# Performance work log

Hardware: AMD Instinct MI355X
Metric: run time of the kernel (lower is better)

The kernel has to match this reference:

```python
import jax, jax.numpy as jnp
import numpy as np

N = 1_000_000
H = 128
G = 4096


def setup_inputs() -> dict:
    key = jax.random.key(0)
    k1, k2, k3, k4 = jax.random.split(key, 4)
    x = jax.random.normal(k1, (N, H), dtype=jnp.float32)
    batch = jnp.sort(jax.random.randint(k2, (N,), 0, G, dtype=jnp.int64))
    w1 = jax.random.normal(k3, (H, H), dtype=jnp.float32) * 0.05
    b1 = jnp.zeros((H,), dtype=jnp.float32)
    w2 = jax.random.normal(k4, (H, 1), dtype=jnp.float32) * 0.05
    b2 = jnp.zeros((1,), dtype=jnp.float32)
    return {"x": x, "batch": batch, "w1": w1, "b1": b1, "w2": w2, "b2": b2, "num_graphs": G}


def reference(x, batch, w1, b1, w2, b2, num_graphs):
    # attention MLP: Linear -> Tanh -> Linear(->1)
    s = (jnp.tanh(x @ w1 + b1) @ w2 + b2)[:, 0]  # [N]
    # segmented (per-graph) stable softmax
    smax = jax.ops.segment_max(s, batch, num_segments=num_graphs)  # [G]
    smax = jnp.where(jnp.isfinite(smax), smax, 0.0)  # guard empty graphs
    e = jnp.exp(s - smax[batch])  # [N]
    denom = jax.ops.segment_sum(e, batch, num_segments=num_graphs)  # [G]
    w = e / jnp.where(denom > 0, denom, 1.0)[batch]  # [N]
    # weighted sum pooling per graph -> [G, H]
    pooled = jax.ops.segment_sum(x * w[:, None], batch, num_segments=num_graphs)
    return pooled
```

## Files before the change

kernel.cpp:

```cpp
#include <hip/hip_runtime.h>
#include <math.h>

#define H 128

typedef float f32x4 __attribute__((ext_vector_type(4)));
typedef __bf16 bf16x8 __attribute__((ext_vector_type(8)));

__device__ __forceinline__ float fast_tanh(float v) {
    float e = __expf(2.0f * v);
    float r = __builtin_amdgcn_rcpf(e + 1.0f);
    return fmaf(-2.0f, r, 1.0f);
}

__global__ __launch_bounds__(512, 4) void k_compute_s_mfma(
    const float* __restrict__ x, const float* __restrict__ w1,
    const float* __restrict__ b1, const float* __restrict__ w2,
    const float* __restrict__ b2, float* __restrict__ s, int n, int ntiles)
{
    __shared__ __bf16 wsm[2 * H * H];

    const int tid = threadIdx.x;

    for (int idx = tid; idx < H * H; idx += 512) {
        int k = idx >> 7, nn = idx & 127;
        float v = w1[idx];
        __bf16 h = (__bf16)v;
        __bf16 l = (__bf16)(v - (float)h);
        int c = (k >> 3) ^ (nn & 15);
        int pos = nn * H + c * 8 + (k & 7);
        wsm[pos] = h;
        wsm[H * H + pos] = l;
    }

    const int wv = tid >> 6;
    const int lane = tid & 63;
    const int p = lane & 15;
    const int q = lane >> 4;
    const float b2v = b2[0];

    __syncthreads();

    for (int tile = blockIdx.x; tile < ntiles; tile += (int)gridDim.x) {
        const long long base = (long long)tile * 256 + wv * 32;

        bf16x8 ah[2][4], al[2][4];
        #pragma unroll
        for (int mt = 0; mt < 2; ++mt) {
            long long r = base + mt * 16 + p;
            const float4* rp = (const float4*)(x + r * H);
            const bool ok = (r < (long long)n);
            #pragma unroll
            for (int kc = 0; kc < 4; ++kc) {
                float4 u0 = {0.f, 0.f, 0.f, 0.f}, u1 = {0.f, 0.f, 0.f, 0.f};
                if (ok) { u0 = rp[kc * 8 + q * 2]; u1 = rp[kc * 8 + q * 2 + 1]; }
                float vals[8] = {u0.x, u0.y, u0.z, u0.w, u1.x, u1.y, u1.z, u1.w};
                #pragma unroll
                for (int j = 0; j < 8; ++j) {
                    __bf16 h = (__bf16)vals[j];
                    ah[mt][kc][j] = h;
                    al[mt][kc][j] = (__bf16)(vals[j] - (float)h);
                }
            }
        }

        float part[2][4] = {{0.f, 0.f, 0.f, 0.f}, {0.f, 0.f, 0.f, 0.f}};

        #pragma unroll
        for (int nt = 0; nt < 8; ++nt) {
            const int nn = nt * 16 + p;
            f32x4 acc0 = {0.f, 0.f, 0.f, 0.f};
            f32x4 acc1 = {0.f, 0.f, 0.f, 0.f};
            #pragma unroll
            for (int kc = 0; kc < 4; ++kc) {
                const int c = (kc * 4 + q) ^ p;
                const __bf16* bb = &wsm[nn * H + c * 8];
                bf16x8 bh = *(const bf16x8*)bb;
                bf16x8 bl = *(const bf16x8*)(bb + H * H);
                acc0 = __builtin_amdgcn_mfma_f32_16x16x32_bf16(ah[0][kc], bh, acc0, 0, 0, 0);
                acc1 = __builtin_amdgcn_mfma_f32_16x16x32_bf16(ah[1][kc], bh, acc1, 0, 0, 0);
                acc0 = __builtin_amdgcn_mfma_f32_16x16x32_bf16(al[0][kc], bh, acc0, 0, 0, 0);
                acc1 = __builtin_amdgcn_mfma_f32_16x16x32_bf16(al[1][kc], bh, acc1, 0, 0, 0);
                acc0 = __builtin_amdgcn_mfma_f32_16x16x32_bf16(ah[0][kc], bl, acc0, 0, 0, 0);
                acc1 = __builtin_amdgcn_mfma_f32_16x16x32_bf16(ah[1][kc], bl, acc1, 0, 0, 0);
            }
            const float b1v = b1[nn];
            const float w2v = w2[nn];
            #pragma unroll
            for (int rg = 0; rg < 4; ++rg) {
                part[0][rg] = fmaf(fast_tanh(acc0[rg] + b1v), w2v, part[0][rg]);
                part[1][rg] = fmaf(fast_tanh(acc1[rg] + b1v), w2v, part[1][rg]);
            }
        }

        #pragma unroll
        for (int off = 1; off < 16; off <<= 1) {
            #pragma unroll
            for (int mt = 0; mt < 2; ++mt)
                #pragma unroll
                for (int rg = 0; rg < 4; ++rg)
                    part[mt][rg] += __shfl_xor(part[mt][rg], off);
        }
        if (p == 0) {
            #pragma unroll
            for (int mt = 0; mt < 2; ++mt)
                #pragma unroll
                for (int rg = 0; rg < 4; ++rg) {
                    long long row = base + mt * 16 + q * 4 + rg;
                    if (row < (long long)n) s[row] = part[mt][rg] + b2v;
                }
        }
    }
}

__global__ void k_offsets(const int* __restrict__ batch, int n, int g_count,
                          int* __restrict__ offs)
{
    int g = blockIdx.x * blockDim.x + threadIdx.x;
    if (g > g_count) return;
    const bool is64 = (batch[n - 1] == 0);
    int lo = 0, hi = n;
    while (lo < hi) {
        int mid = (lo + hi) >> 1;
        int v = is64 ? batch[2 * mid] : batch[mid];
        if (v < g) lo = mid + 1; else hi = mid;
    }
    offs[g] = lo;
}

__global__ __launch_bounds__(256) void k_stats_pool(
    const float* __restrict__ x, const float* __restrict__ s,
    const int* __restrict__ offs, float* __restrict__ out)
{
    const int g = blockIdx.x;
    const int tid = threadIdx.x;
    const int start = offs[g], end = offs[g + 1];

    __shared__ float redm[4], redd[4];
    __shared__ float4 red[8][32];

    float m = -INFINITY;
    for (int i = start + tid; i < end; i += 256) m = fmaxf(m, s[i]);
    #pragma unroll
    for (int off = 32; off; off >>= 1) m = fmaxf(m, __shfl_xor(m, off));
    if ((tid & 63) == 0) redm[tid >> 6] = m;
    __syncthreads();
    m = fmaxf(fmaxf(redm[0], redm[1]), fmaxf(redm[2], redm[3]));
    if (!(m >= -3.0e38f)) m = 0.0f;

    float d = 0.0f;
    for (int i = start + tid; i < end; i += 256) d += __expf(s[i] - m);
    #pragma unroll
    for (int off = 32; off; off >>= 1) d += __shfl_xor(d, off);
    if ((tid & 63) == 0) redd[tid >> 6] = d;
    __syncthreads();
    d = redd[0] + redd[1] + redd[2] + redd[3];
    const float inv = (d > 0.0f) ? (1.0f / d) : 1.0f;

    const int rr = tid >> 5;
    const int c4 = tid & 31;
    float4 acc = {0.f, 0.f, 0.f, 0.f};
    #pragma unroll 2
    for (int i = start + rr; i < end; i += 8) {
        float w = __expf(s[i] - m) * inv;
        float4 xv = ((const float4*)(x + (size_t)i * H))[c4];
        acc.x = fmaf(w, xv.x, acc.x);
        acc.y = fmaf(w, xv.y, acc.y);
        acc.z = fmaf(w, xv.z, acc.z);
        acc.w = fmaf(w, xv.w, acc.w);
    }
    red[rr][c4] = acc;
    __syncthreads();
    if (rr == 0) {
        float4 t = red[0][c4];
        #pragma unroll
        for (int j = 1; j < 8; ++j) {
            float4 u = red[j][c4];
            t.x += u.x; t.y += u.y; t.z += u.z; t.w += u.w;
        }
        ((float4*)(out + (size_t)g * H))[c4] = t;
    }
}

extern "C" void kernel_launch(void* const* d_in, const int* in_sizes, int n_in,
                              void* d_out, int out_size, void* d_ws, size_t ws_size,
                              hipStream_t stream)
{
    const float* x     = (const float*)d_in[0];
    const int*   batch = (const int*)d_in[1];
    const float* w1    = (const float*)d_in[2];
    const float* b1    = (const float*)d_in[3];
    const float* w2    = (const float*)d_in[4];
    const float* b2    = (const float*)d_in[5];
    const int n = in_sizes[0] / H;
    const int G = out_size / H;
    float* out = (float*)d_out;

    float* s    = (float*)d_ws;
    int*   offs = (int*)(s + n);

    const int tiles = (n + 255) / 256;
    k_compute_s_mfma<<<1024, 512, 0, stream>>>(x, w1, b1, w2, b2, s, n, tiles);
    k_offsets<<<(G + 1 + 255) / 256, 256, 0, stream>>>(batch, n, G, offs);
    k_stats_pool<<<G, 256, 0, stream>>>(x, s, offs, out);
}
```

Baseline: 1.207 ms.

## Fuse segment softmax pooling into the MLP score kernel using atomics

The score kernel now also computes exp(score) and the weighted pooling in the same pass, so x is no longer read a second time and the separate offsets and stats passes go away. Each wave loops over the distinct graph ids among its rows, reducing partial sums with shuffles and then adding them into the output and a denominator buffer with atomics. A small kernel zeroes those buffers first and another divides by the denominator at the end. The per-graph max subtraction and b2 are dropped because softmax does not change under a constant shift, which risks overflow for large scores. Pooled x is rebuilt from its split bf16 hi/lo parts, and the launch bound moves to 2 blocks per CU.

```diff
diff --git a/kernel.cpp b/kernel.cpp
--- a/kernel.cpp
+++ b/kernel.cpp
@@ -12,10 +12,11 @@
     return fmaf(-2.0f, r, 1.0f);
 }
 
-__global__ __launch_bounds__(512, 4) void k_compute_s_mfma(
-    const float* __restrict__ x, const float* __restrict__ w1,
-    const float* __restrict__ b1, const float* __restrict__ w2,
-    const float* __restrict__ b2, float* __restrict__ s, int n, int ntiles)
+__global__ __launch_bounds__(512, 2) void k_fused(
+    const float* __restrict__ x, const int* __restrict__ batch,
+    const float* __restrict__ w1, const float* __restrict__ b1,
+    const float* __restrict__ w2, float* __restrict__ out,
+    float* __restrict__ denom, int n, int ntiles)
 {
     __shared__ __bf16 wsm[2 * H * H];
 
@@ -36,7 +37,8 @@
     const int lane = tid & 63;
     const int p = lane & 15;
     const int q = lane >> 4;
-    const float b2v = b2[0];
+
+    const bool is64 = (batch[n - 1] == 0);
 
     __syncthreads();
 
@@ -44,15 +46,16 @@
         const long long base = (long long)tile * 256 + wv * 32;
 
         bf16x8 ah[2][4], al[2][4];
+        bool okm[2];
         #pragma unroll
         for (int mt = 0; mt < 2; ++mt) {
             long long r = base + mt * 16 + p;
             const float4* rp = (const float4*)(x + r * H);
-            const bool ok = (r < (long long)n);
+            okm[mt] = (r < (long long)n);
             #pragma unroll
             for (int kc = 0; kc < 4; ++kc) {
                 float4 u0 = {0.f, 0.f, 0.f, 0.f}, u1 = {0.f, 0.f, 0.f, 0.f};
-                if (ok) { u0 = rp[kc * 8 + q * 2]; u1 = rp[kc * 8 + q * 2 + 1]; }
+                if (okm[mt]) { u0 = rp[kc * 8 + q * 2]; u1 = rp[kc * 8 + q * 2 + 1]; }
                 float vals[8] = {u0.x, u0.y, u0.z, u0.w, u1.x, u1.y, u1.z, u1.w};
                 #pragma unroll
                 for (int j = 0; j < 8; ++j) {
@@ -100,85 +103,86 @@
                 for (int rg = 0; rg < 4; ++rg)
                     part[mt][rg] += __shfl_xor(part[mt][rg], off);
         }
-        if (p == 0) {
-            #pragma unroll
-            for (int mt = 0; mt < 2; ++mt)
-                #pragma unroll
-                for (int rg = 0; rg < 4; ++rg) {
-                    long long row = base + mt * 16 + q * 4 + rg;
-                    if (row < (long long)n) s[row] = part[mt][rg] + b2v;
+
+        float e[2];
+        #pragma unroll
+        for (int mt = 0; mt < 2; ++mt) {
+            const int srcl = (p >> 2) * 16;
+            float a0 = __shfl(part[mt][0], srcl);
+            float a1 = __shfl(part[mt][1], srcl);
+            float a2 = __shfl(part[mt][2], srcl);
+            float a3 = __shfl(part[mt][3], srcl);
+            int rs = p & 3;
+            float sv = (rs == 0) ? a0 : (rs == 1) ? a1 : (rs == 2) ? a2 : a3;
+            e[mt] = okm[mt] ? __expf(sv) : 0.0f;
+        }
+
+        long long r0 = base + p, r1 = base + 16 + p;
+        int ga = okm[0] ? (is64 ? batch[(size_t)r0 * 2] : batch[r0]) : 0x7FFFFFFF;
+        int gb = okm[1] ? (is64 ? batch[(size_t)r1 * 2] : batch[r1]) : 0x7FFFFFFF;
+
+        while (true) {
+            int gm = min(ga, gb);
+            #pragma unroll
+            for (int off = 1; off < 16; off <<= 1)
+                gm = min(gm, __shfl_xor(gm, off));
+            if (gm == 0x7FFFFFFF) break;
+
+            float ea = (ga == gm) ? e[0] : 0.0f;
+            float eb = (gb == gm) ? e[1] : 0.0f;
+
+            float dsum = ea + eb;
+            #pragma unroll
+            for (int off = 1; off < 16; off <<= 1)
+                dsum += __shfl_xor(dsum, off);
+            if (lane == 0) atomicAdd(&denom[gm], dsum);
+
+            #pragma unroll
+            for (int kc = 0; kc < 4; ++kc) {
+                float t[8];
+                #pragma unroll
+                for (int j = 0; j < 8; ++j)
+                    t[j] = ea * ((float)ah[0][kc][j] + (float)al[0][kc][j])
+                         + eb * ((float)ah[1][kc][j] + (float)al[1][kc][j]);
+                #pragma unroll
+                for (int off = 1; off < 16; off <<= 1) {
+                    #pragma unroll
+                    for (int j = 0; j < 8; ++j)
+                        t[j] += __shfl_xor(t[j], off);
                 }
+                if (p == 0) {
+                    float* ob = out + (size_t)gm * H + kc * 32 + q * 8;
+                    #pragma unroll
+                    for (int j = 0; j < 8; ++j)
+                        atomicAdd(&ob[j], t[j]);
+                }
+            }
+
+            if (ga == gm) ga = 0x7FFFFFFF;
+            if (gb == gm) gb = 0x7FFFFFFF;
         }
     }
 }
 
-__global__ void k_offsets(const int* __restrict__ batch, int n, int g_count,
-                          int* __restrict__ offs)
-{
-    int g = blockIdx.x * blockDim.x + threadIdx.x;
-    if (g > g_count) return;
-    const bool is64 = (batch[n - 1] == 0);
-    int lo = 0, hi = n;
-    while (lo < hi) {
-        int mid = (lo + hi) >> 1;
-        int v = is64 ? batch[2 * mid] : batch[mid];
-        if (v < g) lo = mid + 1; else hi = mid;
-    }
-    offs[g] = lo;
-}
-
-__global__ __launch_bounds__(256) void k_stats_pool(
-    const float* __restrict__ x, const float* __restrict__ s,
-    const int* __restrict__ offs, float* __restrict__ out)
-{
-    const int g = blockIdx.x;
-    const int tid = threadIdx.x;
-    const int start = offs[g], end = offs[g + 1];
-
-    __shared__ float redm[4], redd[4];
-    __shared__ float4 red[8][32];
-
-    float m = -INFINITY;
-    for (int i = start + tid; i < end; i += 256) m = fmaxf(m, s[i]);
-    #pragma unroll
-    for (int off = 32; off; off >>= 1) m = fmaxf(m, __shfl_xor(m, off));
-    if ((tid & 63) == 0) redm[tid >> 6] = m;
-    __syncthreads();
-    m = fmaxf(fmaxf(redm[0], redm[1]), fmaxf(redm[2], redm[3]));
-    if (!(m >= -3.0e38f)) m = 0.0f;
-
-    float d = 0.0f;
-    for (int i = start + tid; i < end; i += 256) d += __expf(s[i] - m);
-    #pragma unroll
-    for (int off = 32; off; off >>= 1) d += __shfl_xor(d, off);
-    if ((tid & 63) == 0) redd[tid >> 6] = d;
-    __syncthreads();
-    d = redd[0] + redd[1] + redd[2] + redd[3];
-    const float inv = (d > 0.0f) ? (1.0f / d) : 1.0f;
-
-    const int rr = tid >> 5;
-    const int c4 = tid & 31;
-    float4 acc = {0.f, 0.f, 0.f, 0.f};
-    #pragma unroll 2
-    for (int i = start + rr; i < end; i += 8) {
-        float w = __expf(s[i] - m) * inv;
-        float4 xv = ((const float4*)(x + (size_t)i * H))[c4];
-        acc.x = fmaf(w, xv.x, acc.x);
-        acc.y = fmaf(w, xv.y, acc.y);
-        acc.z = fmaf(w, xv.z, acc.z);
-        acc.w = fmaf(w, xv.w, acc.w);
-    }
-    red[rr][c4] = acc;
-    __syncthreads();
-    if (rr == 0) {
-        float4 t = red[0][c4];
-        #pragma unroll
-        for (int j = 1; j < 8; ++j) {
-            float4 u = red[j][c4];
-            t.x += u.x; t.y += u.y; t.z += u.z; t.w += u.w;
-        }
-        ((float4*)(out + (size_t)g * H))[c4] = t;
-    }
+__global__ void k_zero(float* __restrict__ out, float* __restrict__ denom,
+                       int nf, int g_count)
+{
+    int i = blockIdx.x * blockDim.x + threadIdx.x;
+    if (i < nf) out[i] = 0.0f;
+    else if (i < nf + g_count) denom[i - nf] = 0.0f;
+}
+
+__global__ void k_norm(float* __restrict__ out, const float* __restrict__ denom,
+                       int total4)
+{
+    int i = blockIdx.x * blockDim.x + threadIdx.x;
+    if (i >= total4) return;
+    int g = i >> 5;
+    float d = denom[g];
+    float inv = (d > 0.0f) ? (1.0f / d) : 1.0f;
+    float4 v = ((float4*)out)[i];
+    v.x *= inv; v.y *= inv; v.z *= inv; v.w *= inv;
+    ((float4*)out)[i] = v;
 }
 
 extern "C" void kernel_launch(void* const* d_in, const int* in_sizes, int n_in,
@@ -190,16 +194,15 @@
     const float* w1    = (const float*)d_in[2];
     const float* b1    = (const float*)d_in[3];
     const float* w2    = (const float*)d_in[4];
-    const float* b2    = (const float*)d_in[5];
     const int n = in_sizes[0] / H;
     const int G = out_size / H;
     float* out = (float*)d_out;
 
-    float* s    = (float*)d_ws;
-    int*   offs = (int*)(s + n);
-
+    float* denom = (float*)d_ws;
+
+    const int nf = G * H;
     const int tiles = (n + 255) / 256;
-    k_compute_s_mfma<<<1024, 512, 0, stream>>>(x, w1, b1, w2, b2, s, n, tiles);
-    k_offsets<<<(G + 1 + 255) / 256, 256, 0, stream>>>(batch, n, G, offs);
-    k_stats_pool<<<G, 256, 0, stream>>>(x, s, offs, out);
-}
+    k_zero<<<(nf + G + 255) / 256, 256, 0, stream>>>(out, denom, nf, G);
+    k_fused<<<1024, 512, 0, stream>>>(x, batch, w1, b1, w2, out, denom, n, tiles);
+    k_norm<<<(G * 32 + 255) / 256, 256, 0, stream>>>(out, denom, G * 32);
+}
```

After: 1.202 ms. Within noise of the previous version (-0.4%).
